# Kernel optimization log

Hardware: AMD Instinct MI355X
Metric: run time of the kernel (lower is better)

## Reference

```python
import jax, jax.numpy as jnp
import numpy as np

B, F, H = 512, 64, 256
INPUT_LEN, TARGET_LEN = 128, 128


def _gru_step(h, xt, Wih, Whh, bih, bhh):
    # PyTorch GRU cell: gates ordered [r, z, n]
    gi = xt @ Wih.T + bih            # [B, 3H]
    gh = h @ Whh.T + bhh             # [B, 3H]
    ir, iz, inn = jnp.split(gi, 3, axis=-1)
    hr, hz, hn = jnp.split(gh, 3, axis=-1)
    r = jax.nn.sigmoid(ir + hr)
    z = jax.nn.sigmoid(iz + hz)
    n = jnp.tanh(inn + r * hn)
    return (1.0 - z) * n + z * h


def setup_inputs() -> dict:
    key = jax.random.key(0)
    ks = jax.random.split(key, 12)
    s_in = 1.0 / np.sqrt(H)
    x = jax.random.normal(ks[0], (B, INPUT_LEN + TARGET_LEN, F), dtype=jnp.float32)
    u = lambda k, shp: jax.random.uniform(k, shp, jnp.float32, -s_in, s_in)
    return {
        "x": x,
        "enc_Wih": u(ks[1], (3 * H, F)), "enc_Whh": u(ks[2], (3 * H, H)),
        "enc_bih": u(ks[3], (3 * H,)), "enc_bhh": u(ks[4], (3 * H,)),
        "dec_Wih": u(ks[5], (3 * H, F)), "dec_Whh": u(ks[6], (3 * H, H)),
        "dec_bih": u(ks[7], (3 * H,)), "dec_bhh": u(ks[8], (3 * H,)),
        "reg_W": u(ks[9], (F, H)), "reg_b": u(ks[10], (F,)),
        "input_len": INPUT_LEN, "target_len": TARGET_LEN,
    }


def reference(x, enc_Wih, enc_Whh, enc_bih, enc_bhh,
              dec_Wih, dec_Whh, dec_bih, dec_bhh,
              reg_W, reg_b, input_len, target_len):
    source_seq = x[:, :input_len, :]                       # [B, Tin, F]
    b = source_seq.shape[0]

    # Encoder GRU over source sequence, h0 = 0
    def enc_step(h, xt):
        h = _gru_step(h, xt, enc_Wih, enc_Whh, enc_bih, enc_bhh)
        return h, None
    h0 = jnp.zeros((b, enc_Whh.shape[1]), dtype=x.dtype)
    h_enc, _ = jax.lax.scan(enc_step, h0, source_seq.transpose(1, 0, 2))

    # Decoder: eval mode -> teacher forcing prob 0, always feed back own output
    dec_in0 = source_seq[:, -1, :]                         # [B, F]
    def dec_step(carry, _):
        h, inp = carry
        h = _gru_step(h, inp, dec_Wih, dec_Whh, dec_bih, dec_bhh)
        out = h @ reg_W.T + reg_b                          # [B, F]
        return (h, out), out
    (_, _), outs = jax.lax.scan(dec_step, (h_enc, dec_in0), None, length=target_len)
    return outs.transpose(1, 0, 2)                         # [B, Tout, F]
```

## Files before the change

kernel.cpp:

```cpp
#include <hip/hip_runtime.h>
#include <math.h>

#define Bsz 512
#define Fsz 64
#define Hsz 256
#define TSTEPS 128
#define G3 768

#define BG 16
#define HB 16
#define NBLK 256
#define NTHR 256

#define RED_SLOTS 40
#define OFF_B (RED_SLOTS*64*16)
#define SMEM_BYTES (OFF_B + 512)

typedef float f32x4 __attribute__((ext_vector_type(4)));
typedef short s16x8 __attribute__((ext_vector_type(8)));
typedef unsigned int  u32x4 __attribute__((ext_vector_type(4)));

#define MF(a,b,c) __builtin_amdgcn_mfma_f32_16x16x32_bf16(a,b,c,0,0,0)

static __device__ __forceinline__ unsigned short bf16_rne(float f){
    union { float f; unsigned u; } v; v.f = f;
    return (unsigned short)((v.u + 0x7FFFu + ((v.u >> 16) & 1u)) >> 16);
}
static __device__ __forceinline__ float bf16_to_f(unsigned short h){
    union { unsigned u; float f; } v; v.u = ((unsigned)h) << 16; return v.f;
}
static __device__ __forceinline__ void split8(const float* p, s16x8& hi, s16x8& lo){
    #pragma unroll
    for (int t = 0; t < 8; ++t){
        float f = p[t];
        unsigned short h = bf16_rne(f);
        hi[t] = (short)h;
        lo[t] = (short)bf16_rne(f - bf16_to_f(h));
    }
}
static __device__ __forceinline__ float sigmoidf_(float v){ return 1.0f/(1.0f + expf(-v)); }

__device__ __forceinline__ u32x4 load_sys_b128u(const unsigned* p){
    u32x4 r;
    asm volatile("global_load_dwordx4 %0, %1, off sc0 sc1" : "=v"(r) : "v"(p) : "memory");
    return r;
}
__device__ __forceinline__ unsigned load_sys_b32u_nw(const unsigned* p){
    unsigned r;
    asm volatile("global_load_dword %0, %1, off sc0 sc1" : "=v"(r) : "v"(p) : "memory");
    return r;
}
__device__ __forceinline__ void store_sys_b32u(unsigned* p, unsigned v){
    asm volatile("global_store_dword %0, %1, off sc0 sc1" :: "v"(p), "v"(v) : "memory");
}
__device__ __forceinline__ int load_sys_i32(const int* p){
    int r;
    asm volatile("global_load_dword %0, %1, off sc0 sc1\n\ts_waitcnt vmcnt(0)"
                 : "=v"(r) : "v"(p) : "memory");
    return r;
}
__device__ __forceinline__ void waitcnt0(){ asm volatile("s_waitcnt vmcnt(0)" ::: "memory"); }
__device__ __forceinline__ void regbar(u32x4& v){ asm volatile("" : "+v"(v)); }
__device__ __forceinline__ void regbar32(unsigned& v){ asm volatile("" : "+v"(v)); }

static __device__ __forceinline__ void unpack8(const u32x4 a, const u32x4 b, s16x8& hi, s16x8& lo){
    #pragma unroll
    for (int e = 0; e < 4; ++e){
        hi[e]   = (short)(a[e] >> 16);  lo[e]   = (short)(a[e] & 0xFFFFu);
        hi[4+e] = (short)(b[e] >> 16);  lo[4+e] = (short)(b[e] & 0xFFFFu);
    }
}

extern "C" __global__ void gru_setup(const float* __restrict__ x,
                                     const float* __restrict__ dWih,
                                     const float* __restrict__ dbih,
                                     const float* __restrict__ regW,
                                     const float* __restrict__ regb,
                                     float* __restrict__ Mw,
                                     float* __restrict__ cfold,
                                     float* __restrict__ gi0)
{
    int idx = blockIdx.x*blockDim.x + threadIdx.x;
    if (idx < G3*Hsz) {
        int g = idx >> 8, j = idx & 255;
        float a = 0.f;
        #pragma unroll 8
        for (int f = 0; f < Fsz; ++f) a += dWih[g*Fsz + f]*regW[f*Hsz + j];
        Mw[idx] = a;
    } else if (idx < G3*Hsz + G3) {
        int g = idx - G3*Hsz;
        float a = dbih[g];
        #pragma unroll 8
        for (int f = 0; f < Fsz; ++f) a += dWih[g*Fsz + f]*regb[f];
        cfold[g] = a;
    } else {
        int e = idx - (G3*Hsz + G3);
        if (e < Bsz*G3) {
            int b = e / G3, g = e - b*G3;
            const float* xp = x + (size_t)b*(256*64) + 127*64;
            float a = dbih[g];
            #pragma unroll 8
            for (int f = 0; f < Fsz; ++f) a += xp[f]*dWih[g*Fsz + f];
            gi0[e] = a;
        }
    }
}

extern "C" __global__ void __launch_bounds__(NTHR, 1)
gru_persistent(const float* __restrict__ x,
               const float* __restrict__ eWih, const float* __restrict__ eWhh,
               const float* __restrict__ ebih, const float* __restrict__ ebhh,
               const float* __restrict__ dWhh, const float* __restrict__ dbhh,
               const float* __restrict__ Mw,   const float* __restrict__ cfold,
               const float* __restrict__ gi0,  const float* __restrict__ regW,
               const float* __restrict__ regb,
               unsigned* __restrict__ hbuf, unsigned* __restrict__ canary,
               float* __restrict__ out)
{
    extern __shared__ char lds[];
    f32x4* s_redv = (f32x4*)lds;
    float* s_bias = (float*)(lds + OFF_B);
    float* s_dbh  = s_bias + 64;
    float* s_b3   = s_bias + 112;

    const int tid  = threadIdx.x;
    const int wv   = tid >> 6;
    const int lane = tid & 63;
    const int quad = lane >> 4;
    const int lcol = lane & 15;
    const int bg   = blockIdx.x & 15;
    const int hb   = blockIdx.x >> 4;
    const int hcol = hb*16 + lcol;
    const int mw   = wv & 1;
    const int kh   = wv >> 1;
    const int jb   = kh*2;
    const int hr0  = mw*16 + quad*4 + jb;
    const f32x4 z4 = {0.f, 0.f, 0.f, 0.f};

    unsigned* mycan = canary + ((size_t)bg*64 + hb*4 + wv)*4;
    const int* canp = (const int*)canary + ((size_t)bg*64 + lane)*4;
    const int  can_mine = ((lane >> 2) == hb);

    s16x8 wfh[3][2], wfl[3][2];
    s16x8 ufh[3], ufl[3];
    s16x8 rwh[2], rwl[2];
    #pragma unroll
    for (int g = 0; g < 3; ++g){
        #pragma unroll
        for (int q = 0; q < 2; ++q)
            split8(eWhh + (size_t)(g*256 + hcol)*256 + wv*64 + q*32 + quad*8,
                   wfh[g][q], wfl[g][q]);
        split8(eWih + (size_t)(g*256 + hcol)*64 + kh*32 + quad*8, ufh[g], ufl[g]);
    }
    if (tid < 16){
        int c = hb*16 + tid;
        s_bias[tid]    = ebih[c]       + ebhh[c];
        s_bias[16+tid] = ebih[256+c]   + ebhh[256+c];
        s_bias[32+tid] = ebih[512+c];
        s_bias[48+tid] = ebhh[512+c];
    }
    __syncthreads();

    for (int g = 0; g <= 2*TSTEPS; ++g){
        const bool enc  = (g < TSTEPS);
        const bool last = (g == 2*TSTEPS);
        const unsigned* hin = hbuf + (size_t)(g & 1)*Bsz*Hsz;
        unsigned* hout = hbuf + (size_t)((g+1) & 1)*Bsz*Hsz;

        if (g == TSTEPS){
            #pragma unroll
            for (int gg = 0; gg < 3; ++gg)
                #pragma unroll
                for (int q = 0; q < 2; ++q)
                    split8(dWhh + (size_t)(gg*256 + hcol)*256 + wv*64 + q*32 + quad*8,
                           wfh[gg][q], wfl[gg][q]);
            #pragma unroll
            for (int q = 0; q < 2; ++q){
                split8(Mw   + (size_t)(2*256 + hcol)*256 + wv*64 + q*32 + quad*8,
                       ufh[q], ufl[q]);
                split8(regW + (size_t)(hb*4 + (lcol & 3))*256 + wv*64 + q*32 + quad*8,
                       rwh[q], rwl[q]);
            }
            if (tid < 16){
                int c = hb*16 + tid;
                s_bias[tid]    = cfold[c]     + dbhh[c];
                s_bias[16+tid] = cfold[256+c] + dbhh[256+c];
                s_bias[32+tid] = cfold[512+c];
                s_dbh[tid]     = dbhh[c];
                s_dbh[16+tid]  = dbhh[256+c];
                s_dbh[32+tid]  = dbhh[512+c];
            }
            if (tid < 4) s_b3[tid] = regb[hb*4 + tid];
            __syncthreads();
        }
        if (g == TSTEPS + 1){
            #pragma unroll
            for (int gg = 0; gg < 2; ++gg)
                #pragma unroll
                for (int q = 0; q < 2; ++q){
                    float tmp[8];
                    const float* pa = dWhh + (size_t)(gg*256 + hcol)*256 + wv*64 + q*32 + quad*8;
                    const float* pb = Mw   + (size_t)(gg*256 + hcol)*256 + wv*64 + q*32 + quad*8;
                    #pragma unroll
                    for (int t2 = 0; t2 < 8; ++t2) tmp[t2] = pa[t2] + pb[t2];
                    split8(tmp, wfh[gg][q], wfl[gg][q]);
                }
        }

        f32x4 aR[2], aZ[2], aNi[2], aNh[2], oa[2];
        oa[0] = z4; oa[1] = z4;
        if (wv == 0 && !last){
            if (g == TSTEPS){
                #pragma unroll
                for (int m = 0; m < 2; ++m)
                    #pragma unroll
                    for (int j = 0; j < 4; ++j){
                        int grow_ = bg*32 + m*16 + quad*4 + j;
                        const float* gp = gi0 + (size_t)grow_*G3 + hcol;
                        aR[m][j]  = gp[0]   + s_dbh[lcol];
                        aZ[m][j]  = gp[256] + s_dbh[16+lcol];
                        aNi[m][j] = gp[512];
                        aNh[m][j] = s_dbh[32+lcol];
                    }
            } else {
                float bR = s_bias[lcol], bZ = s_bias[16+lcol], bNi = s_bias[32+lcol];
                float bNh = enc ? s_bias[48+lcol] : s_dbh[32+lcol];
                #pragma unroll
                for (int m = 0; m < 2; ++m){
                    aR[m] = (f32x4){bR,bR,bR,bR}; aZ[m] = (f32x4){bZ,bZ,bZ,bZ};
                    aNi[m] = (f32x4){bNi,bNi,bNi,bNi}; aNh[m] = (f32x4){bNh,bNh,bNh,bNh};
                }
            }
        } else {
            #pragma unroll
            for (int m = 0; m < 2; ++m){ aR[m]=z4; aZ[m]=z4; aNi[m]=z4; aNh[m]=z4; }
        }

        f32x4 xv0, xv1;
        if (enc){
            const float* xp = x + (size_t)(bg*32 + mw*16 + lcol)*(256*64)
                                + (size_t)g*64 + kh*32 + quad*8;
            xv0 = *(const f32x4*)xp;
            xv1 = *(const f32x4*)(xp + 4);
        }

        if (g){
            while (1){
                int v = load_sys_i32(canp);
                if (__all(can_mine | (v >= g))) break;
                __builtin_amdgcn_s_sleep(1);
            }
        }

        const unsigned* ab = hin + (size_t)(bg*32 + lcol)*256 + wv*64 + quad*8;
        u32x4 t[8];
        #pragma unroll
        for (int m = 0; m < 2; ++m)
            #pragma unroll
            for (int q = 0; q < 2; ++q)
                #pragma unroll
                for (int h4 = 0; h4 < 2; ++h4)
                    t[m*4+q*2+h4] = load_sys_b128u(ab + m*4096 + q*32 + h4*4);
        const unsigned* hoA = hin + (size_t)(bg*32 + hr0)*256 + hcol;
        unsigned ho0 = load_sys_b32u_nw(hoA);
        unsigned ho1 = load_sys_b32u_nw(hoA + 256);

        if (enc){
            float xf[8];
            #pragma unroll
            for (int e = 0; e < 4; ++e){ xf[e] = xv0[e]; xf[4+e] = xv1[e]; }
            s16x8 xh, xl;
            split8(xf, xh, xl);
            #define XMF(M) { \
                aR[M] =MF(xh,ufh[0],aR[M]);  aR[M] =MF(xh,ufl[0],aR[M]);  aR[M] =MF(xl,ufh[0],aR[M]);  \
                aZ[M] =MF(xh,ufh[1],aZ[M]);  aZ[M] =MF(xh,ufl[1],aZ[M]);  aZ[M] =MF(xl,ufh[1],aZ[M]);  \
                aNi[M]=MF(xh,ufh[2],aNi[M]); aNi[M]=MF(xh,ufl[2],aNi[M]); aNi[M]=MF(xl,ufh[2],aNi[M]); }
            if (mw == 0) XMF(0) else XMF(1)
            #undef XMF
        }

        waitcnt0();
        #pragma unroll
        for (int jj = 0; jj < 8; ++jj) regbar(t[jj]);
        regbar32(ho0); regbar32(ho1);

        #pragma unroll
        for (int m = 0; m < 2; ++m){
            #pragma unroll
            for (int q = 0; q < 2; ++q){
                s16x8 ah, al;
                unpack8(t[m*4+q*2], t[m*4+q*2+1], ah, al);
                if (!last){
                    aR[m]=MF(ah,wfh[0][q],aR[m]); aR[m]=MF(ah,wfl[0][q],aR[m]); aR[m]=MF(al,wfh[0][q],aR[m]);
                    aZ[m]=MF(ah,wfh[1][q],aZ[m]); aZ[m]=MF(ah,wfl[1][q],aZ[m]); aZ[m]=MF(al,wfh[1][q],aZ[m]);
                    aNh[m]=MF(ah,wfh[2][q],aNh[m]); aNh[m]=MF(ah,wfl[2][q],aNh[m]); aNh[m]=MF(al,wfh[2][q],aNh[m]);
                    if (!enc && g > TSTEPS){
                        aNi[m]=MF(ah,ufh[q],aNi[m]); aNi[m]=MF(ah,ufl[q],aNi[m]); aNi[m]=MF(al,ufh[q],aNi[m]);
                    }
                }
                if (g >= TSTEPS + 1){
                    oa[m]=MF(ah,rwh[q],oa[m]); oa[m]=MF(ah,rwl[q],oa[m]); oa[m]=MF(al,rwh[q],oa[m]);
                }
            }
        }

        if (!last){
            f32x4* rp = s_redv + (size_t)(wv*8)*64 + lane;
            rp[0]   = aR[0]; rp[64]  = aZ[0]; rp[128] = aNi[0]; rp[192] = aNh[0];
            rp[256] = aR[1]; rp[320] = aZ[1]; rp[384] = aNi[1]; rp[448] = aNh[1];
        }
        if (g >= TSTEPS + 1){
            f32x4* op = s_redv + (size_t)(32 + wv*2)*64 + lane;
            op[0] = oa[0]; op[64] = oa[1];
        }
        __syncthreads();

        if (!last){
            f32x4 R = z4, Z = z4, Ni = z4, Nh = z4;
            #pragma unroll
            for (int w2 = 0; w2 < 4; ++w2){
                const f32x4* rp = s_redv + (size_t)(w2*8 + mw*4)*64 + lane;
                R += rp[0]; Z += rp[64]; Ni += rp[128]; Nh += rp[192];
            }
            #define EW(J, HW, RO) { \
                float r = sigmoidf_(R[J]); \
                float z = sigmoidf_(Z[J]); \
                float n = tanhf(Ni[J] + r*Nh[J]); \
                float hold = bf16_to_f((unsigned short)((HW) >> 16)) \
                           + bf16_to_f((unsigned short)((HW) & 0xFFFFu)); \
                float hv = (1.0f - z)*n + z*hold; \
                unsigned short p1 = bf16_rne(hv); \
                unsigned short p0 = bf16_rne(hv - bf16_to_f(p1)); \
                store_sys_b32u(hout + (size_t)(bg*32 + hr0 + RO)*256 + hcol, \
                               (((unsigned)p1) << 16) | (unsigned)p0); }
            if (jb == 0){ EW(0, ho0, 0); EW(1, ho1, 1); }
            else        { EW(2, ho0, 0); EW(3, ho1, 1); }
            #undef EW
        }

        if (g >= TSTEPS + 1 && wv >= 2){
            const int m2 = wv - 2;
            float b3 = s_b3[lcol & 3];
            f32x4 ot = {b3, b3, b3, b3};
            #pragma unroll
            for (int w2 = 0; w2 < 4; ++w2)
                ot += s_redv[(size_t)(32 + w2*2 + m2)*64 + lane];
            if (lcol < 4){
                const int oidx = g - TSTEPS - 1;
                #pragma unroll
                for (int j = 0; j < 4; ++j)
                    out[(size_t)(bg*32 + m2*16 + quad*4 + j)*(TSTEPS*Fsz)
                        + (size_t)oidx*Fsz + hb*4 + lcol] = ot[j];
            }
        }

        if (!last){
            waitcnt0();
            if (lane == 0) store_sys_b32u(mycan, (unsigned)(g + 1));
        }
        __syncthreads();
    }
}

extern "C" void kernel_launch(void* const* d_in, const int* in_sizes, int n_in,
                              void* d_out, int out_size, void* d_ws, size_t ws_size,
                              hipStream_t stream)
{
    (void)in_sizes; (void)n_in; (void)out_size; (void)ws_size;
    const float* x    = (const float*)d_in[0];
    const float* eWih = (const float*)d_in[1];
    const float* eWhh = (const float*)d_in[2];
    const float* ebih = (const float*)d_in[3];
    const float* ebhh = (const float*)d_in[4];
    const float* dWih = (const float*)d_in[5];
    const float* dWhh = (const float*)d_in[6];
    const float* dbih = (const float*)d_in[7];
    const float* dbhh = (const float*)d_in[8];
    const float* regW = (const float*)d_in[9];
    const float* regb = (const float*)d_in[10];
    float* out = (float*)d_out;

    unsigned* hbuf = (unsigned*)d_ws;
    float* Mw    = (float*)d_ws + 2*Bsz*Hsz;
    float* gi0   = Mw + G3*Hsz;
    float* cfold = gi0 + Bsz*G3;
    unsigned* canary = (unsigned*)(cfold + 1024);

    hipMemsetAsync(hbuf, 0, (size_t)Bsz*Hsz*sizeof(unsigned), stream);
    hipMemsetAsync(canary, 0, (size_t)BG*64*4*sizeof(unsigned), stream);

    hipLaunchKernelGGL(gru_setup, dim3(2307), dim3(256), 0, stream,
                       x, dWih, dbih, regW, regb, Mw, cfold, gi0);

    hipFuncSetAttribute((const void*)gru_persistent,
                        hipFuncAttributeMaxDynamicSharedMemorySize, SMEM_BYTES);

    void* args[] = { (void*)&x, (void*)&eWih, (void*)&eWhh, (void*)&ebih, (void*)&ebhh,
                     (void*)&dWhh, (void*)&dbhh, (void*)&Mw, (void*)&cfold, (void*)&gi0,
                     (void*)&regW, (void*)&regb, (void*)&hbuf, (void*)&canary, (void*)&out };
    hipError_t rc = hipLaunchCooperativeKernel((const void*)gru_persistent,
                                               dim3(NBLK), dim3(NTHR), args,
                                               SMEM_BYTES, stream);
    if (rc != hipSuccess) {
        hipLaunchKernelGGL(gru_persistent, dim3(NBLK), dim3(NTHR), SMEM_BYTES, stream,
                           x, eWih, eWhh, ebih, ebhh, dWhh, dbhh, Mw, cfold, gi0,
                           regW, regb, hbuf, canary, out);
    }
}
```

Before: 1.162 ms.

## Embed step tags in hidden-state words to skip flag polling, use fast transcendentals

The two lowest bits of each stored hidden-state word now carry a step tag, so consumers load h optimistically and proceed when all tags match. Only when a tag is stale do they fall back to polling the per-block canary flags and reloading the missing chunks. The canary store moves to right after the h stores, without the trailing waitcnt. Sigmoid and tanh are rewritten with hardware exp2 and rcp intrinsics. In exchange, two bits of low-part precision in the bf16 split are lost and the second buffer is initialised to a non-matching tag.

```diff
diff --git a/kernel.cpp b/kernel.cpp
--- a/kernel.cpp
+++ b/kernel.cpp
@@ -38,7 +38,12 @@
         lo[t] = (short)bf16_rne(f - bf16_to_f(h));
     }
 }
-static __device__ __forceinline__ float sigmoidf_(float v){ return 1.0f/(1.0f + expf(-v)); }
+static __device__ __forceinline__ float sigmoidf_(float v){
+    return __builtin_amdgcn_rcpf(1.0f + __builtin_amdgcn_exp2f(-1.44269504f*v));
+}
+static __device__ __forceinline__ float tanhf_(float v){
+    return 1.0f - 2.0f*__builtin_amdgcn_rcpf(1.0f + __builtin_amdgcn_exp2f(2.88539008f*v));
+}
 
 __device__ __forceinline__ u32x4 load_sys_b128u(const unsigned* p){
     u32x4 r;
@@ -138,8 +143,9 @@
     const f32x4 z4 = {0.f, 0.f, 0.f, 0.f};
 
     unsigned* mycan = canary + ((size_t)bg*64 + hb*4 + wv)*4;
-    const int* canp = (const int*)canary + ((size_t)bg*64 + lane)*4;
-    const int  can_mine = ((lane >> 2) == hb);
+    const int fidx  = wv*16 + (lane & 15);
+    const int* fp   = (const int*)canary + ((size_t)bg*64 + fidx)*4;
+    const int fmine = ((fidx >> 2) == hb);
 
     s16x8 wfh[3][2], wfl[3][2];
     s16x8 ufh[3], ufl[3];
@@ -164,6 +170,8 @@
     for (int g = 0; g <= 2*TSTEPS; ++g){
         const bool enc  = (g < TSTEPS);
         const bool last = (g == 2*TSTEPS);
+        const unsigned tag  = (unsigned)((g >> 1) & 3);
+        const unsigned otag = (unsigned)(((g+1) >> 1) & 3);
         const unsigned* hin = hbuf + (size_t)(g & 1)*Bsz*Hsz;
         unsigned* hout = hbuf + (size_t)((g+1) & 1)*Bsz*Hsz;
 
@@ -244,14 +252,6 @@
             xv1 = *(const f32x4*)(xp + 4);
         }
 
-        if (g){
-            while (1){
-                int v = load_sys_i32(canp);
-                if (__all(can_mine | (v >= g))) break;
-                __builtin_amdgcn_s_sleep(1);
-            }
-        }
-
         const unsigned* ab = hin + (size_t)(bg*32 + lcol)*256 + wv*64 + quad*8;
         u32x4 t[8];
         #pragma unroll
@@ -279,10 +279,52 @@
             #undef XMF
         }
 
-        waitcnt0();
-        #pragma unroll
-        for (int jj = 0; jj < 8; ++jj) regbar(t[jj]);
-        regbar32(ho0); regbar32(ho1);
+        #define UPD() { \
+            _Pragma("unroll") \
+            for (int jj = 0; jj < 8; ++jj) \
+                if (!((done >> jj) & 1u)) \
+                    if (((t[jj][0]&3u)==tag) && ((t[jj][1]&3u)==tag) && \
+                        ((t[jj][2]&3u)==tag) && ((t[jj][3]&3u)==tag)) done |= (1u << jj); \
+            if (!((done >> 8) & 1u) && ((ho0 & 3u) == tag)) done |= 0x100u; \
+            if (!((done >> 9) & 1u) && ((ho1 & 3u) == tag)) done |= 0x200u; }
+
+        {
+            unsigned done = 0;
+            waitcnt0();
+            #pragma unroll
+            for (int jj = 0; jj < 8; ++jj) regbar(t[jj]);
+            regbar32(ho0); regbar32(ho1);
+            UPD();
+            if (!__all((int)(done == 0x3FFu))){
+                while (1){
+                    int v = load_sys_i32(fp);
+                    if (__all(fmine | (v >= g))) break;
+                    __builtin_amdgcn_s_sleep(1);
+                }
+                while (1){
+                    #pragma unroll
+                    for (int m = 0; m < 2; ++m)
+                        #pragma unroll
+                        for (int q = 0; q < 2; ++q)
+                            #pragma unroll
+                            for (int h4 = 0; h4 < 2; ++h4){
+                                const int jj = m*4+q*2+h4;
+                                if (!((done >> jj) & 1u))
+                                    t[jj] = load_sys_b128u(ab + m*4096 + q*32 + h4*4);
+                            }
+                    if (!((done >> 8) & 1u)) ho0 = load_sys_b32u_nw(hoA);
+                    if (!((done >> 9) & 1u)) ho1 = load_sys_b32u_nw(hoA + 256);
+                    waitcnt0();
+                    #pragma unroll
+                    for (int jj = 0; jj < 8; ++jj) regbar(t[jj]);
+                    regbar32(ho0); regbar32(ho1);
+                    UPD();
+                    if (__all((int)(done == 0x3FFu))) break;
+                    __builtin_amdgcn_s_sleep(1);
+                }
+            }
+        }
+        #undef UPD
 
         #pragma unroll
         for (int m = 0; m < 2; ++m){
@@ -325,17 +367,18 @@
             #define EW(J, HW, RO) { \
                 float r = sigmoidf_(R[J]); \
                 float z = sigmoidf_(Z[J]); \
-                float n = tanhf(Ni[J] + r*Nh[J]); \
+                float n = tanhf_(Ni[J] + r*Nh[J]); \
                 float hold = bf16_to_f((unsigned short)((HW) >> 16)) \
                            + bf16_to_f((unsigned short)((HW) & 0xFFFFu)); \
                 float hv = (1.0f - z)*n + z*hold; \
                 unsigned short p1 = bf16_rne(hv); \
                 unsigned short p0 = bf16_rne(hv - bf16_to_f(p1)); \
                 store_sys_b32u(hout + (size_t)(bg*32 + hr0 + RO)*256 + hcol, \
-                               (((unsigned)p1) << 16) | (unsigned)p0); }
+                               (((unsigned)p1) << 16) | ((unsigned)(p0 & 0xFFFCu)) | otag); }
             if (jb == 0){ EW(0, ho0, 0); EW(1, ho1, 1); }
             else        { EW(2, ho0, 0); EW(3, ho1, 1); }
             #undef EW
+            if (lane == 0) store_sys_b32u(mycan, (unsigned)(g + 1));
         }
 
         if (g >= TSTEPS + 1 && wv >= 2){
@@ -352,11 +395,6 @@
                     out[(size_t)(bg*32 + m2*16 + quad*4 + j)*(TSTEPS*Fsz)
                         + (size_t)oidx*Fsz + hb*4 + lcol] = ot[j];
             }
-        }
-
-        if (!last){
-            waitcnt0();
-            if (lane == 0) store_sys_b32u(mycan, (unsigned)(g + 1));
         }
         __syncthreads();
     }
@@ -387,6 +425,7 @@
     unsigned* canary = (unsigned*)(cfold + 1024);
 
     hipMemsetAsync(hbuf, 0, (size_t)Bsz*Hsz*sizeof(unsigned), stream);
+    hipMemsetAsync(hbuf + (size_t)Bsz*Hsz, 3, (size_t)Bsz*Hsz*sizeof(unsigned), stream);
     hipMemsetAsync(canary, 0, (size_t)BG*64*4*sizeof(unsigned), stream);
 
     hipLaunchKernelGGL(gru_setup, dim3(2307), dim3(256), 0, stream,
```

Measured after the change: 1.081 ms. 1.08x faster.

## Split hidden state into hi/lo planes with parity-tagged data validation

Applied to the files above, without the earlier changes.

Stores the recurrent hidden state as separate bf16 hi and lo planes and embeds a one-bit step parity tag in the LSB of each value. Consumers validate the tag and re-poll only the fragments that are stale. The change also double-buffers the LDS reduction area so the trailing per-step __syncthreads can be dropped. Canary flags are published right after the hidden-state stores instead of after the output write, and sigmoid/tanh use fast exp2/rcp intrinsics. The intent is to shorten the cross-block synchronization critical path per timestep. The cost is lost precision from the stolen mantissa bit and more complex polling logic with memory-ordering risk.

```diff
diff --git a/kernel.cpp b/kernel.cpp
--- a/kernel.cpp
+++ b/kernel.cpp
@@ -11,14 +11,14 @@
 #define HB 16
 #define NBLK 256
 #define NTHR 256
+#define PL (Bsz*Hsz)
 
 #define RED_SLOTS 40
-#define OFF_B (RED_SLOTS*64*16)
+#define OFF_B (2*RED_SLOTS*64*16)
 #define SMEM_BYTES (OFF_B + 512)
 
 typedef float f32x4 __attribute__((ext_vector_type(4)));
 typedef short s16x8 __attribute__((ext_vector_type(8)));
-typedef unsigned int  u32x4 __attribute__((ext_vector_type(4)));
 
 #define MF(a,b,c) __builtin_amdgcn_mfma_f32_16x16x32_bf16(a,b,c,0,0,0)
 
@@ -38,38 +38,38 @@
         lo[t] = (short)bf16_rne(f - bf16_to_f(h));
     }
 }
-static __device__ __forceinline__ float sigmoidf_(float v){ return 1.0f/(1.0f + expf(-v)); }
-
-__device__ __forceinline__ u32x4 load_sys_b128u(const unsigned* p){
-    u32x4 r;
+static __device__ __forceinline__ float sigmoidf_(float v){
+    return __builtin_amdgcn_rcpf(1.0f + __builtin_amdgcn_exp2f(-1.44269504f*v));
+}
+static __device__ __forceinline__ float tanhf_(float v){
+    return 1.0f - 2.0f*__builtin_amdgcn_rcpf(1.0f + __builtin_amdgcn_exp2f(2.88539008f*v));
+}
+
+__device__ __forceinline__ s16x8 load_sys_frag(const unsigned short* p){
+    s16x8 r;
     asm volatile("global_load_dwordx4 %0, %1, off sc0 sc1" : "=v"(r) : "v"(p) : "memory");
     return r;
 }
-__device__ __forceinline__ unsigned load_sys_b32u_nw(const unsigned* p){
+__device__ __forceinline__ unsigned load_sys_u16(const unsigned short* p){
     unsigned r;
-    asm volatile("global_load_dword %0, %1, off sc0 sc1" : "=v"(r) : "v"(p) : "memory");
+    asm volatile("global_load_ushort %0, %1, off sc0 sc1" : "=v"(r) : "v"(p) : "memory");
     return r;
+}
+__device__ __forceinline__ void store_sys_b16(unsigned short* p, unsigned v){
+    asm volatile("global_store_short %0, %1, off sc0 sc1" :: "v"(p), "v"(v) : "memory");
 }
 __device__ __forceinline__ void store_sys_b32u(unsigned* p, unsigned v){
     asm volatile("global_store_dword %0, %1, off sc0 sc1" :: "v"(p), "v"(v) : "memory");
 }
-__device__ __forceinline__ int load_sys_i32(const int* p){
+__device__ __forceinline__ int load_flag(const int* p){
     int r;
     asm volatile("global_load_dword %0, %1, off sc0 sc1\n\ts_waitcnt vmcnt(0)"
                  : "=v"(r) : "v"(p) : "memory");
     return r;
 }
 __device__ __forceinline__ void waitcnt0(){ asm volatile("s_waitcnt vmcnt(0)" ::: "memory"); }
-__device__ __forceinline__ void regbar(u32x4& v){ asm volatile("" : "+v"(v)); }
+__device__ __forceinline__ void regbarh(s16x8& v){ asm volatile("" : "+v"(v)); }
 __device__ __forceinline__ void regbar32(unsigned& v){ asm volatile("" : "+v"(v)); }
-
-static __device__ __forceinline__ void unpack8(const u32x4 a, const u32x4 b, s16x8& hi, s16x8& lo){
-    #pragma unroll
-    for (int e = 0; e < 4; ++e){
-        hi[e]   = (short)(a[e] >> 16);  lo[e]   = (short)(a[e] & 0xFFFFu);
-        hi[4+e] = (short)(b[e] >> 16);  lo[4+e] = (short)(b[e] & 0xFFFFu);
-    }
-}
 
 extern "C" __global__ void gru_setup(const float* __restrict__ x,
                                      const float* __restrict__ dWih,
@@ -114,7 +114,7 @@
                const float* __restrict__ Mw,   const float* __restrict__ cfold,
                const float* __restrict__ gi0,  const float* __restrict__ regW,
                const float* __restrict__ regb,
-               unsigned* __restrict__ hbuf, unsigned* __restrict__ canary,
+               unsigned short* __restrict__ hbuf, unsigned* __restrict__ canary,
                float* __restrict__ out)
 {
     extern __shared__ char lds[];
@@ -138,8 +138,9 @@
     const f32x4 z4 = {0.f, 0.f, 0.f, 0.f};
 
     unsigned* mycan = canary + ((size_t)bg*64 + hb*4 + wv)*4;
-    const int* canp = (const int*)canary + ((size_t)bg*64 + lane)*4;
-    const int  can_mine = ((lane >> 2) == hb);
+    const int fidx  = wv*16 + (lane & 15);
+    const int* fp   = (const int*)canary + ((size_t)bg*64 + fidx)*4;
+    const int fmine = ((fidx >> 2) == hb);
 
     s16x8 wfh[3][2], wfl[3][2];
     s16x8 ufh[3], ufl[3];
@@ -164,8 +165,13 @@
     for (int g = 0; g <= 2*TSTEPS; ++g){
         const bool enc  = (g < TSTEPS);
         const bool last = (g == 2*TSTEPS);
-        const unsigned* hin = hbuf + (size_t)(g & 1)*Bsz*Hsz;
-        unsigned* hout = hbuf + (size_t)((g+1) & 1)*Bsz*Hsz;
+        const int  p    = g & 1;
+        const unsigned tb    = (unsigned)((g >> 1) & 1);
+        const unsigned otagb = (unsigned)(((g+1) >> 1) & 1);
+        const unsigned short* hinH = hbuf + (size_t)(g & 1)*2*PL;
+        const unsigned short* hinL = hinH + PL;
+        unsigned short* houtH = hbuf + (size_t)((g+1) & 1)*2*PL;
+        unsigned short* houtL = houtH + PL;
 
         if (g == TSTEPS){
             #pragma unroll
@@ -236,36 +242,11 @@
             for (int m = 0; m < 2; ++m){ aR[m]=z4; aZ[m]=z4; aNi[m]=z4; aNh[m]=z4; }
         }
 
-        f32x4 xv0, xv1;
         if (enc){
             const float* xp = x + (size_t)(bg*32 + mw*16 + lcol)*(256*64)
                                 + (size_t)g*64 + kh*32 + quad*8;
-            xv0 = *(const f32x4*)xp;
-            xv1 = *(const f32x4*)(xp + 4);
-        }
-
-        if (g){
-            while (1){
-                int v = load_sys_i32(canp);
-                if (__all(can_mine | (v >= g))) break;
-                __builtin_amdgcn_s_sleep(1);
-            }
-        }
-
-        const unsigned* ab = hin + (size_t)(bg*32 + lcol)*256 + wv*64 + quad*8;
-        u32x4 t[8];
-        #pragma unroll
-        for (int m = 0; m < 2; ++m)
-            #pragma unroll
-            for (int q = 0; q < 2; ++q)
-                #pragma unroll
-                for (int h4 = 0; h4 < 2; ++h4)
-                    t[m*4+q*2+h4] = load_sys_b128u(ab + m*4096 + q*32 + h4*4);
-        const unsigned* hoA = hin + (size_t)(bg*32 + hr0)*256 + hcol;
-        unsigned ho0 = load_sys_b32u_nw(hoA);
-        unsigned ho1 = load_sys_b32u_nw(hoA + 256);
-
-        if (enc){
+            f32x4 xv0 = *(const f32x4*)xp;
+            f32x4 xv1 = *(const f32x4*)(xp + 4);
             float xf[8];
             #pragma unroll
             for (int e = 0; e < 4; ++e){ xf[e] = xv0[e]; xf[4+e] = xv1[e]; }
@@ -279,17 +260,72 @@
             #undef XMF
         }
 
-        waitcnt0();
+        if (g){
+            while (1){
+                int v = load_flag(fp);
+                if (__all(fmine | (v >= g))) break;
+            }
+        }
+
+        const size_t fb = (size_t)(bg*32 + lcol)*256 + wv*64 + quad*8;
+        const unsigned short* hoHp = hinH + (size_t)(bg*32 + hr0)*256 + hcol;
+        const unsigned short* hoLp = hinL + (size_t)(bg*32 + hr0)*256 + hcol;
+        s16x8 th[4], tl[4];
         #pragma unroll
-        for (int jj = 0; jj < 8; ++jj) regbar(t[jj]);
-        regbar32(ho0); regbar32(ho1);
+        for (int fi = 0; fi < 4; ++fi){
+            const int m = fi >> 1, q = fi & 1;
+            th[fi] = load_sys_frag(hinH + fb + m*4096 + q*32);
+            tl[fi] = load_sys_frag(hinL + fb + m*4096 + q*32);
+        }
+        unsigned hh0 = load_sys_u16(hoHp), hh1 = load_sys_u16(hoHp + 256);
+        unsigned hl0 = load_sys_u16(hoLp), hl1 = load_sys_u16(hoLp + 256);
+
+        {
+            const unsigned tt = tb * 0x00010001u;
+            unsigned done = 0;
+            #define UPD() { \
+                _Pragma("unroll") \
+                for (int fi = 0; fi < 4; ++fi){ \
+                    if (!((done >> fi) & 1u)){ const unsigned* c = (const unsigned*)&th[fi]; \
+                        if ((((c[0]^tt)|(c[1]^tt)|(c[2]^tt)|(c[3]^tt)) & 0x00010001u) == 0u) done |= (1u<<fi); } \
+                    if (!((done >> (4+fi)) & 1u)){ const unsigned* c = (const unsigned*)&tl[fi]; \
+                        if ((((c[0]^tt)|(c[1]^tt)|(c[2]^tt)|(c[3]^tt)) & 0x00010001u) == 0u) done |= (1u<<(4+fi)); } } \
+                if (!((done>>8)&1u)  && (((hh0^tb)&1u)==0u)) done |= 0x100u; \
+                if (!((done>>9)&1u)  && (((hh1^tb)&1u)==0u)) done |= 0x200u; \
+                if (!((done>>10)&1u) && (((hl0^tb)&1u)==0u)) done |= 0x400u; \
+                if (!((done>>11)&1u) && (((hl1^tb)&1u)==0u)) done |= 0x800u; }
+
+            waitcnt0();
+            #pragma unroll
+            for (int fi = 0; fi < 4; ++fi){ regbarh(th[fi]); regbarh(tl[fi]); }
+            regbar32(hh0); regbar32(hh1); regbar32(hl0); regbar32(hl1);
+            UPD();
+            while (!__all((int)(done == 0xFFFu))){
+                #pragma unroll
+                for (int fi = 0; fi < 4; ++fi){
+                    const int m = fi >> 1, q = fi & 1;
+                    if (!((done >> fi) & 1u))     th[fi] = load_sys_frag(hinH + fb + m*4096 + q*32);
+                    if (!((done >> (4+fi)) & 1u)) tl[fi] = load_sys_frag(hinL + fb + m*4096 + q*32);
+                }
+                if (!((done>>8)&1u))  hh0 = load_sys_u16(hoHp);
+                if (!((done>>9)&1u))  hh1 = load_sys_u16(hoHp + 256);
+                if (!((done>>10)&1u)) hl0 = load_sys_u16(hoLp);
+                if (!((done>>11)&1u)) hl1 = load_sys_u16(hoLp + 256);
+                waitcnt0();
+                #pragma unroll
+                for (int fi = 0; fi < 4; ++fi){ regbarh(th[fi]); regbarh(tl[fi]); }
+                regbar32(hh0); regbar32(hh1); regbar32(hl0); regbar32(hl1);
+                UPD();
+            }
+            #undef UPD
+        }
 
         #pragma unroll
         for (int m = 0; m < 2; ++m){
             #pragma unroll
             for (int q = 0; q < 2; ++q){
-                s16x8 ah, al;
-                unpack8(t[m*4+q*2], t[m*4+q*2+1], ah, al);
+                const s16x8 ah = th[m*2+q];
+                const s16x8 al = tl[m*2+q];
                 if (!last){
                     aR[m]=MF(ah,wfh[0][q],aR[m]); aR[m]=MF(ah,wfl[0][q],aR[m]); aR[m]=MF(al,wfh[0][q],aR[m]);
                     aZ[m]=MF(ah,wfh[1][q],aZ[m]); aZ[m]=MF(ah,wfl[1][q],aZ[m]); aZ[m]=MF(al,wfh[1][q],aZ[m]);
@@ -305,12 +341,12 @@
         }
 
         if (!last){
-            f32x4* rp = s_redv + (size_t)(wv*8)*64 + lane;
+            f32x4* rp = s_redv + ((size_t)p*RED_SLOTS + wv*8)*64 + lane;
             rp[0]   = aR[0]; rp[64]  = aZ[0]; rp[128] = aNi[0]; rp[192] = aNh[0];
             rp[256] = aR[1]; rp[320] = aZ[1]; rp[384] = aNi[1]; rp[448] = aNh[1];
         }
         if (g >= TSTEPS + 1){
-            f32x4* op = s_redv + (size_t)(32 + wv*2)*64 + lane;
+            f32x4* op = s_redv + ((size_t)p*RED_SLOTS + 32 + wv*2)*64 + lane;
             op[0] = oa[0]; op[64] = oa[1];
         }
         __syncthreads();
@@ -319,23 +355,23 @@
             f32x4 R = z4, Z = z4, Ni = z4, Nh = z4;
             #pragma unroll
             for (int w2 = 0; w2 < 4; ++w2){
-                const f32x4* rp = s_redv + (size_t)(w2*8 + mw*4)*64 + lane;
+                const f32x4* rp = s_redv + ((size_t)p*RED_SLOTS + w2*8 + mw*4)*64 + lane;
                 R += rp[0]; Z += rp[64]; Ni += rp[128]; Nh += rp[192];
             }
-            #define EW(J, HW, RO) { \
+            #define EW(J, HH, HL, RO) { \
                 float r = sigmoidf_(R[J]); \
                 float z = sigmoidf_(Z[J]); \
-                float n = tanhf(Ni[J] + r*Nh[J]); \
-                float hold = bf16_to_f((unsigned short)((HW) >> 16)) \
-                           + bf16_to_f((unsigned short)((HW) & 0xFFFFu)); \
+                float n = tanhf_(Ni[J] + r*Nh[J]); \
+                float hold = bf16_to_f((unsigned short)(HH)) + bf16_to_f((unsigned short)(HL)); \
                 float hv = (1.0f - z)*n + z*hold; \
-                unsigned short p1 = bf16_rne(hv); \
-                unsigned short p0 = bf16_rne(hv - bf16_to_f(p1)); \
-                store_sys_b32u(hout + (size_t)(bg*32 + hr0 + RO)*256 + hcol, \
-                               (((unsigned)p1) << 16) | (unsigned)p0); }
-            if (jb == 0){ EW(0, ho0, 0); EW(1, ho1, 1); }
-            else        { EW(2, ho0, 0); EW(3, ho1, 1); }
+                unsigned short p1 = (unsigned short)((bf16_rne(hv) & 0xFFFEu) | otagb); \
+                unsigned short p0 = (unsigned short)((bf16_rne(hv - bf16_to_f(p1)) & 0xFFFEu) | otagb); \
+                store_sys_b16(houtH + (size_t)(bg*32 + hr0 + RO)*256 + hcol, (unsigned)p1); \
+                store_sys_b16(houtL + (size_t)(bg*32 + hr0 + RO)*256 + hcol, (unsigned)p0); }
+            if (jb == 0){ EW(0, hh0, hl0, 0); EW(1, hh1, hl1, 1); }
+            else        { EW(2, hh0, hl0, 0); EW(3, hh1, hl1, 1); }
             #undef EW
+            if (lane == 0) store_sys_b32u(mycan, (unsigned)(g + 1));
         }
 
         if (g >= TSTEPS + 1 && wv >= 2){
@@ -344,7 +380,7 @@
             f32x4 ot = {b3, b3, b3, b3};
             #pragma unroll
             for (int w2 = 0; w2 < 4; ++w2)
-                ot += s_redv[(size_t)(32 + w2*2 + m2)*64 + lane];
+                ot += s_redv[((size_t)p*RED_SLOTS + 32 + w2*2 + m2)*64 + lane];
             if (lcol < 4){
                 const int oidx = g - TSTEPS - 1;
                 #pragma unroll
@@ -353,12 +389,6 @@
                         + (size_t)oidx*Fsz + hb*4 + lcol] = ot[j];
             }
         }
-
-        if (!last){
-            waitcnt0();
-            if (lane == 0) store_sys_b32u(mycan, (unsigned)(g + 1));
-        }
-        __syncthreads();
     }
 }
 
@@ -380,13 +410,14 @@
     const float* regb = (const float*)d_in[10];
     float* out = (float*)d_out;
 
-    unsigned* hbuf = (unsigned*)d_ws;
+    unsigned short* hbuf = (unsigned short*)d_ws;
     float* Mw    = (float*)d_ws + 2*Bsz*Hsz;
     float* gi0   = Mw + G3*Hsz;
-    float* cfold = gi0 + Bsz*G3;
+    float* cfold = gi0 + (size_t)Bsz*G3;
     unsigned* canary = (unsigned*)(cfold + 1024);
 
-    hipMemsetAsync(hbuf, 0, (size_t)Bsz*Hsz*sizeof(unsigned), stream);
+    hipMemsetAsync(hbuf, 0, (size_t)2*PL*sizeof(unsigned short), stream);
+    hipMemsetAsync(hbuf + (size_t)2*PL, 3, (size_t)2*PL*sizeof(unsigned short), stream);
     hipMemsetAsync(canary, 0, (size_t)BG*64*4*sizeof(unsigned), stream);
 
     hipLaunchKernelGGL(gru_setup, dim3(2307), dim3(256), 0, stream,
```

Measured after the change: 1.099 ms. 1.06x faster.
